# Performance work log

Hardware: AMD Instinct MI355X
Metric: run time of the kernel (lower is better)

The kernel has to match this reference:

```python
import jax, jax.numpy as jnp
import numpy as np

C = 512        # num_channels
HEADS = 8      # num_channels // num_head_channels
DH = 64        # num_head_channels
G = 32         # num_groups
EPS = 1e-5
SCALE = DH ** -0.25  # pre-multiplied into q and k (scale applied twice -> 1/sqrt(DH))


def setup_inputs() -> dict:
    key = jax.random.key(0)
    ks = jax.random.split(key, 10)
    B, H, W = 2, 64, 64
    def w(k):
        return jax.random.normal(k, (C, C), jnp.float32) * 0.02
    def b(k):
        return jax.random.normal(k, (C,), jnp.float32) * 0.02
    return {
        "x": jax.random.normal(ks[0], (B, C, H, W), jnp.float32),
        "gn_w": jnp.ones((C,), jnp.float32),
        "gn_b": jnp.zeros((C,), jnp.float32),
        "wq": w(ks[1]), "bq": b(ks[2]),
        "wk": w(ks[3]), "bk": b(ks[4]),
        "wv": w(ks[5]), "bv": b(ks[6]),
        "wp": w(ks[7]), "bp": b(ks[8]),
    }


def reference(x, gn_w, gn_b, wq, bq, wk, bk, wv, bv, wp, bp):
    B, Cc, H, W = x.shape
    # GroupNorm over (C/G, H, W) per group
    xr = x.reshape(B, G, Cc // G, H * W)
    mean = xr.mean(axis=(2, 3), keepdims=True)
    var = xr.var(axis=(2, 3), keepdims=True)
    h = ((xr - mean) * jax.lax.rsqrt(var + EPS)).reshape(B, Cc, H, W)
    h = h * gn_w[None, :, None, None] + gn_b[None, :, None, None]
    # B C H W -> B (H W) C
    t = h.reshape(B, Cc, H * W).transpose(0, 2, 1)
    # q/k pre-multiplied by SCALE (equivalent to pre_multiply_weights_by_scale)
    q = (t @ wq.T + bq) * SCALE
    k = (t @ wk.T + bk) * SCALE
    v = t @ wv.T + bv
    def split_heads(a):  # B HW (h d) -> B h HW d
        return a.reshape(B, H * W, HEADS, DH).transpose(0, 2, 1, 3)
    q, k, v = split_heads(q), split_heads(k), split_heads(v)
    # full HWxHW score matrix, softmax over keys
    attn = jax.nn.softmax(jnp.einsum('bhqd,bhkd->bhqk', q, k), axis=-1)
    o = jnp.einsum('bhqk,bhkd->bhqd', attn, v)
    o = o.transpose(0, 2, 1, 3).reshape(B, H * W, Cc)  # join heads
    o = o @ wp.T + bp
    # B (H W) C -> B C H W, residual
    return o.transpose(0, 2, 1).reshape(B, Cc, H, W) + x
```

## Files before the change

kernel.cpp:

```cpp
#include <hip/hip_runtime.h>

#define HWN 4096
#define CCH 512
#define NHEAD 8
#define DHD 64
#define NBATCH 2
#define QK_SCALE 0.35355339059327373f
#define LOG2E    1.4426950408889634f

using floatx4 = __attribute__((ext_vector_type(4))) float;
using bf16x8  = __attribute__((ext_vector_type(8))) short;
using bf16x4  = __attribute__((ext_vector_type(4))) short;

__device__ __forceinline__ unsigned short f2b(float f) {
  union { float f; unsigned u; } x; x.f = f;
  unsigned r = x.u + 0x7FFFu + ((x.u >> 16) & 1u);
  return (unsigned short)(r >> 16);
}

__device__ __forceinline__ float fast_exp2(float x) {
#if __has_builtin(__builtin_amdgcn_exp2f)
  return __builtin_amdgcn_exp2f(x);
#else
  return __expf(x * 0.69314718056f);
#endif
}

__device__ __forceinline__ unsigned pack_bf16_trunc(float lo, float hi) {
  return __builtin_amdgcn_perm(__float_as_uint(hi), __float_as_uint(lo), 0x07060302u);
}

__global__ __launch_bounds__(256) void gn_stats(const float* __restrict__ x,
                                                float* __restrict__ stat) {
  int bg = blockIdx.x;
  const float4* p = (const float4*)(x + (size_t)bg * 65536) + blockIdx.y * 2048;
  float s = 0.f, ss = 0.f;
  for (int i = threadIdx.x; i < 2048; i += 256) {
    float4 v = p[i];
    s  += v.x + v.y + v.z + v.w;
    ss += v.x*v.x + v.y*v.y + v.z*v.z + v.w*v.w;
  }
  for (int off = 32; off; off >>= 1) {
    s  += __shfl_xor(s, off);
    ss += __shfl_xor(ss, off);
  }
  __shared__ float red[8];
  int w = threadIdx.x >> 6;
  if ((threadIdx.x & 63) == 0) { red[w] = s; red[4 + w] = ss; }
  __syncthreads();
  if (threadIdx.x == 0) {
    float S  = red[0] + red[1] + red[2] + red[3];
    float SS = red[4] + red[5] + red[6] + red[7];
    atomicAdd(&stat[bg], S);
    atomicAdd(&stat[64 + bg], SS);
  }
}

__global__ __launch_bounds__(256) void prep_w(
    const float* __restrict__ wq, const float* __restrict__ wk,
    const float* __restrict__ wv, const float* __restrict__ wp,
    const float* __restrict__ bq, const float* __restrict__ bk,
    const float* __restrict__ bv,
    unsigned short* __restrict__ Wqkv, unsigned short* __restrict__ Wp,
    float* __restrict__ bqkv) {
  int i = blockIdx.x * 256 + threadIdx.x;
  if (i < 786432) {
    int row = i >> 9;
    float v;
    if (row < 512)       v = wq[i] * (QK_SCALE * LOG2E);
    else if (row < 1024) v = wk[i - 262144] * QK_SCALE;
    else                 v = wv[i - 524288];
    Wqkv[i] = f2b(v);
  } else if (i < 1048576) {
    Wp[i - 786432] = f2b(wp[i - 786432]);
  } else if (i < 1050112) {
    int j = i - 1048576;
    float v = (j < 512) ? bq[j] * (QK_SCALE * LOG2E)
            : (j < 1024) ? bk[j - 512] * QK_SCALE
            : bv[j - 1024];
    bqkv[j] = v;
  }
}

__global__ __launch_bounds__(256) void gn_apply(
    const float* __restrict__ x, const float* __restrict__ stat,
    const float* __restrict__ gnw, const float* __restrict__ gnb,
    unsigned short* __restrict__ t) {
  int pt = blockIdx.x & 63;
  int ct = (blockIdx.x >> 6) & 7;
  int b  = blockIdx.x >> 9;
  int c0 = ct * 64, p0 = pt * 64;
  __shared__ float tile[64][68];
  int tid = threadIdx.x;
  for (int pp = 0; pp < 4; ++pp) {
    int f = (pp * 256 + tid) * 4;
    int cl = f >> 6, pl = f & 63;
    int c = c0 + cl;
    float4 v = *(const float4*)(x + ((size_t)(b * 512 + c)) * 4096 + p0 + pl);
    int g = c >> 4;
    float S    = stat[b * 32 + g];
    float SS   = stat[64 + b * 32 + g];
    float mean = S * (1.f / 65536.f);
    float var  = SS * (1.f / 65536.f) - mean * mean;
    float rstd = rsqrtf(var + 1e-5f);
    float w  = gnw[c] * rstd;
    float bb = gnb[c] - mean * w;
    tile[cl][pl + 0] = v.x * w + bb;
    tile[cl][pl + 1] = v.y * w + bb;
    tile[cl][pl + 2] = v.z * w + bb;
    tile[cl][pl + 3] = v.w * w + bb;
  }
  __syncthreads();
  for (int pp = 0; pp < 2; ++pp) {
    int f = (pp * 256 + tid) * 8;
    int pl = f >> 6, cl = f & 63;
    unsigned short u[8];
#pragma unroll
    for (int j = 0; j < 8; ++j) u[j] = f2b(tile[cl + j][pl]);
    *(uint4*)(t + ((size_t)(b * 4096 + p0 + pl)) * 512 + c0 + cl) = *(uint4*)u;
  }
}

__global__ __launch_bounds__(256) void gemm_qkv(
    const unsigned short* __restrict__ t, const unsigned short* __restrict__ Wqkv,
    const float* __restrict__ bqkv,
    unsigned short* __restrict__ qo, unsigned short* __restrict__ ko,
    unsigned short* __restrict__ vo) {
  int M0 = blockIdx.x * 64;
  int N0 = blockIdx.y * 64;
  __shared__ unsigned short At[64][72];
  __shared__ unsigned short Bt[64][72];
  int tid = threadIdx.x, w = tid >> 6, l = tid & 63;
  int quad = l >> 4, m16 = l & 15;
  floatx4 acc[4] = {};
  for (int k0 = 0; k0 < 512; k0 += 64) {
    __syncthreads();
#pragma unroll
    for (int pp = 0; pp < 2; ++pp) {
      int f = (pp * 256 + tid) * 8;
      int r = f >> 6, c = f & 63;
      *(uint4*)&At[r][c] = *(const uint4*)(t    + (size_t)(M0 + r) * 512 + k0 + c);
      *(uint4*)&Bt[r][c] = *(const uint4*)(Wqkv + (size_t)(N0 + r) * 512 + k0 + c);
    }
    __syncthreads();
    bf16x8 af0 = *(const bf16x8*)&At[w * 16 + m16][quad * 8];
    bf16x8 af1 = *(const bf16x8*)&At[w * 16 + m16][32 + quad * 8];
#pragma unroll
    for (int nt = 0; nt < 4; ++nt) {
      bf16x8 b0 = *(const bf16x8*)&Bt[nt * 16 + m16][quad * 8];
      bf16x8 b1 = *(const bf16x8*)&Bt[nt * 16 + m16][32 + quad * 8];
      acc[nt] = __builtin_amdgcn_mfma_f32_16x16x32_bf16(af0, b0, acc[nt], 0, 0, 0);
      acc[nt] = __builtin_amdgcn_mfma_f32_16x16x32_bf16(af1, b1, acc[nt], 0, 0, 0);
    }
  }
  int which = N0 >> 9;
  int head  = (N0 & 511) >> 6;
  if (which == 2) {
    __syncthreads();
#pragma unroll
    for (int nt = 0; nt < 4; ++nt) {
      int d = nt * 16 + m16;
      float bias = bqkv[N0 + d];
#pragma unroll
      for (int r = 0; r < 4; ++r)
        At[d][w * 16 + quad * 4 + r] = f2b(acc[nt][r] + bias);
    }
    __syncthreads();
    int bb = M0 >> 12, p0 = M0 & 4095;
    unsigned short* dst = vo + ((size_t)(bb * 8 + head) * 64) * 4096;
#pragma unroll
    for (int pp = 0; pp < 2; ++pp) {
      int f = (pp * 256 + tid) * 8;
      int d = f >> 6, pl = f & 63;
      *(uint4*)(dst + (size_t)d * 4096 + p0 + pl) = *(uint4*)&At[d][pl];
    }
  } else {
    unsigned short* dst = (which == 0) ? qo : ko;
#pragma unroll
    for (int nt = 0; nt < 4; ++nt) {
      int n = N0 + nt * 16 + m16;
      float bias = bqkv[n];
      int d = n & 63;
#pragma unroll
      for (int r = 0; r < 4; ++r) {
        int m = M0 + w * 16 + quad * 4 + r;
        int b = m >> 12, p = m & 4095;
        dst[(((size_t)(b * 8 + head) * 4096 + p) << 6) + d] = f2b(acc[nt][r] + bias);
      }
    }
  }
}

__global__ __launch_bounds__(256, 4) void attn(
    const unsigned short* __restrict__ q, const unsigned short* __restrict__ k,
    const unsigned short* __restrict__ vt, unsigned short* __restrict__ o) {
  int qt = blockIdx.x;
  int bh = blockIdx.y;
  int b = bh >> 3, h = bh & 7;
  __shared__ unsigned short Kt[128][72];
  __shared__ unsigned short Vt[64][136];
  int tid = threadIdx.x, w = tid >> 6, l = tid & 63;
  int quad = l >> 4, m16 = l & 15;
  const size_t base = (size_t)bh * HWN * DHD;
  int krow_base = ((m16 >> 2) * 8) + (m16 & 3);

  bf16x8 qf0, qf1;
  {
    int qrow = qt * 64 + w * 16 + m16;
    const unsigned short* qp = q + base + (size_t)qrow * 64 + quad * 8;
    qf0 = *(const bf16x8*)qp;
    qf1 = *(const bf16x8*)(qp + 32);
  }
  bf16x8 ones;
#pragma unroll
  for (int z = 0; z < 8; ++z) ones[z] = (short)0x3F80;

  floatx4 accO[4] = {};
  floatx4 accL = {};
  float mrow = -1e30f;

  for (int kt = 0; kt < 32; ++kt) {
    __syncthreads();
#pragma unroll
    for (int pp = 0; pp < 4; ++pp) {
      int f = (pp * 256 + tid) * 8;
      int rk = f >> 6, ck = f & 63;
      *(uint4*)&Kt[rk][ck] = *(const uint4*)(k + base + (size_t)(kt * 128 + rk) * 64 + ck);
      int rv = f >> 7, cv = f & 127;
      *(uint4*)&Vt[rv][cv] = *(const uint4*)(vt + base + (size_t)rv * 4096 + kt * 128 + cv);
    }
    __syncthreads();
    floatx4 s[8];
#pragma unroll
    for (int nt = 0; nt < 4; ++nt)
#pragma unroll
      for (int hh = 0; hh < 2; ++hh) {
        int row = nt * 32 + hh * 4 + krow_base;
        bf16x8 kf0 = *(const bf16x8*)&Kt[row][quad * 8];
        bf16x8 kf1 = *(const bf16x8*)&Kt[row][32 + quad * 8];
        floatx4 z = {};
        z = __builtin_amdgcn_mfma_f32_16x16x32_bf16(kf0, qf0, z, 0, 0, 0);
        s[nt * 2 + hh] = __builtin_amdgcn_mfma_f32_16x16x32_bf16(kf1, qf1, z, 0, 0, 0);
      }
    float m0 = fmaxf(fmaxf(s[0][0], s[0][1]), fmaxf(s[0][2], s[0][3]));
    float m1 = fmaxf(fmaxf(s[1][0], s[1][1]), fmaxf(s[1][2], s[1][3]));
    float m2 = fmaxf(fmaxf(s[2][0], s[2][1]), fmaxf(s[2][2], s[2][3]));
    float m3 = fmaxf(fmaxf(s[3][0], s[3][1]), fmaxf(s[3][2], s[3][3]));
    float m4 = fmaxf(fmaxf(s[4][0], s[4][1]), fmaxf(s[4][2], s[4][3]));
    float m5 = fmaxf(fmaxf(s[5][0], s[5][1]), fmaxf(s[5][2], s[5][3]));
    float m6 = fmaxf(fmaxf(s[6][0], s[6][1]), fmaxf(s[6][2], s[6][3]));
    float m7 = fmaxf(fmaxf(s[7][0], s[7][1]), fmaxf(s[7][2], s[7][3]));
    float mx = fmaxf(fmaxf(fmaxf(m0, m1), fmaxf(m2, m3)),
                     fmaxf(fmaxf(m4, m5), fmaxf(m6, m7)));
    mx = fmaxf(mx, __shfl_xor(mx, 16));
    mx = fmaxf(mx, __shfl_xor(mx, 32));
    bool grew = mx > mrow;
    float mnew = fmaxf(mrow, mx);
#pragma unroll
    for (int nt = 0; nt < 8; ++nt)
#pragma unroll
      for (int i = 0; i < 4; ++i)
        s[nt][i] = fast_exp2(s[nt][i] - mnew);
    if (__ballot(grew)) {
      float alpha = fast_exp2(mrow - mnew);
      float al0 = __shfl(alpha, quad * 4 + 0);
      float al1 = __shfl(alpha, quad * 4 + 1);
      float al2 = __shfl(alpha, quad * 4 + 2);
      float al3 = __shfl(alpha, quad * 4 + 3);
#pragma unroll
      for (int dt = 0; dt < 4; ++dt) {
        accO[dt][0] *= al0; accO[dt][1] *= al1;
        accO[dt][2] *= al2; accO[dt][3] *= al3;
      }
      accL[0] *= al0; accL[1] *= al1; accL[2] *= al2; accL[3] *= al3;
    }
    mrow = mnew;
    bf16x8 pf[4];
#pragma unroll
    for (int nt = 0; nt < 4; ++nt) {
      union { unsigned u[4]; bf16x8 v; } pu;
      pu.u[0] = pack_bf16_trunc(s[nt * 2][0],     s[nt * 2][1]);
      pu.u[1] = pack_bf16_trunc(s[nt * 2][2],     s[nt * 2][3]);
      pu.u[2] = pack_bf16_trunc(s[nt * 2 + 1][0], s[nt * 2 + 1][1]);
      pu.u[3] = pack_bf16_trunc(s[nt * 2 + 1][2], s[nt * 2 + 1][3]);
      pf[nt] = pu.v;
    }
#pragma unroll
    for (int dt = 0; dt < 4; ++dt) {
#pragma unroll
      for (int nt = 0; nt < 4; ++nt) {
        bf16x8 vf = *(const bf16x8*)&Vt[dt * 16 + m16][nt * 32 + quad * 8];
        accO[dt] = __builtin_amdgcn_mfma_f32_16x16x32_bf16(pf[nt], vf, accO[dt], 0, 0, 0);
      }
    }
#pragma unroll
    for (int nt = 0; nt < 4; ++nt)
      accL = __builtin_amdgcn_mfma_f32_16x16x32_bf16(pf[nt], ones, accL, 0, 0, 0);
  }
  float li0 = 1.f / accL[0];
  float li1 = 1.f / accL[1];
  float li2 = 1.f / accL[2];
  float li3 = 1.f / accL[3];
#pragma unroll
  for (int dt = 0; dt < 4; ++dt) {
    int d = dt * 16 + m16;
    int qrow = qt * 64 + w * 16 + quad * 4;
    size_t rowb = ((size_t)(b * 4096 + qrow)) * 512 + h * 64 + d;
    o[rowb]           = f2b(accO[dt][0] * li0);
    o[rowb + 512]     = f2b(accO[dt][1] * li1);
    o[rowb + 1024]    = f2b(accO[dt][2] * li2);
    o[rowb + 1536]    = f2b(accO[dt][3] * li3);
  }
}

__global__ __launch_bounds__(256) void gemm_out(
    const unsigned short* __restrict__ o, const unsigned short* __restrict__ Wp,
    const float* __restrict__ bp, const float* __restrict__ x,
    float* __restrict__ out) {
  int C0 = blockIdx.x * 64, P0 = blockIdx.y * 64, b = blockIdx.z;
  __shared__ unsigned short At[64][72];
  __shared__ unsigned short Bt[64][72];
  int tid = threadIdx.x, w = tid >> 6, l = tid & 63;
  int quad = l >> 4, m16 = l & 15;
  floatx4 acc[4] = {};
  for (int k0 = 0; k0 < 512; k0 += 64) {
    __syncthreads();
#pragma unroll
    for (int pp = 0; pp < 2; ++pp) {
      int f = (pp * 256 + tid) * 8;
      int r = f >> 6, c = f & 63;
      *(uint4*)&At[r][c] = *(const uint4*)(Wp + (size_t)(C0 + r) * 512 + k0 + c);
      *(uint4*)&Bt[r][c] = *(const uint4*)(o + ((size_t)(b * 4096 + P0 + r)) * 512 + k0 + c);
    }
    __syncthreads();
    bf16x8 af0 = *(const bf16x8*)&At[w * 16 + m16][quad * 8];
    bf16x8 af1 = *(const bf16x8*)&At[w * 16 + m16][32 + quad * 8];
#pragma unroll
    for (int nt = 0; nt < 4; ++nt) {
      bf16x8 b0 = *(const bf16x8*)&Bt[nt * 16 + m16][quad * 8];
      bf16x8 b1 = *(const bf16x8*)&Bt[nt * 16 + m16][32 + quad * 8];
      acc[nt] = __builtin_amdgcn_mfma_f32_16x16x32_bf16(af0, b0, acc[nt], 0, 0, 0);
      acc[nt] = __builtin_amdgcn_mfma_f32_16x16x32_bf16(af1, b1, acc[nt], 0, 0, 0);
    }
  }
#pragma unroll
  for (int r = 0; r < 4; ++r) {
    int c = C0 + w * 16 + quad * 4 + r;
    float bias = bp[c];
#pragma unroll
    for (int nt = 0; nt < 4; ++nt) {
      int p = P0 + nt * 16 + m16;
      size_t idx = ((size_t)(b * 512 + c)) * 4096 + p;
      out[idx] = acc[nt][r] + bias + x[idx];
    }
  }
}

extern "C" void kernel_launch(void* const* d_in, const int* in_sizes, int n_in,
                              void* d_out, int out_size, void* d_ws, size_t ws_size,
                              hipStream_t stream) {
  const float* x   = (const float*)d_in[0];
  const float* gnw = (const float*)d_in[1];
  const float* gnb = (const float*)d_in[2];
  const float* wq  = (const float*)d_in[3];
  const float* bq  = (const float*)d_in[4];
  const float* wk  = (const float*)d_in[5];
  const float* bk  = (const float*)d_in[6];
  const float* wv  = (const float*)d_in[7];
  const float* bv  = (const float*)d_in[8];
  const float* wp  = (const float*)d_in[9];
  const float* bp  = (const float*)d_in[10];
  float* out = (float*)d_out;

  char* ws = (char*)d_ws;
  float* stat          = (float*)ws;          ws += 1024;
  float* bqkv          = (float*)ws;          ws += 8192;
  unsigned short* Wqkv = (unsigned short*)ws; ws += (size_t)1536 * 512 * 2;
  unsigned short* Wp   = (unsigned short*)ws; ws += (size_t)512 * 512 * 2;
  unsigned short* t    = (unsigned short*)ws; ws += (size_t)8192 * 512 * 2;
  unsigned short* qb   = (unsigned short*)ws; ws += (size_t)8192 * 512 * 2;
  unsigned short* kb   = (unsigned short*)ws; ws += (size_t)8192 * 512 * 2;
  unsigned short* vb   = (unsigned short*)ws; ws += (size_t)8192 * 512 * 2;
  unsigned short* ob   = (unsigned short*)ws; ws += (size_t)8192 * 512 * 2;

  hipMemsetAsync(stat, 0, 512, stream);
  dim3 g0(64, 8);
  gn_stats<<<g0, 256, 0, stream>>>(x, stat);
  prep_w<<<4103, 256, 0, stream>>>(wq, wk, wv, wp, bq, bk, bv, Wqkv, Wp, bqkv);
  gn_apply<<<1024, 256, 0, stream>>>(x, stat, gnw, gnb, t);
  dim3 g1(128, 24);
  gemm_qkv<<<g1, 256, 0, stream>>>(t, Wqkv, bqkv, qb, kb, vb);
  dim3 g2(64, 16);
  attn<<<g2, 256, 0, stream>>>(qb, kb, vb, ob);
  dim3 g3(8, 64, 2);
  gemm_out<<<g3, 256, 0, stream>>>(ob, Wp, bp, x, out);
}
```

Baseline: 274.4 us.

## Process two 16-row query tiles per wave in attention kernel

Each wave in the attention kernel now handles 32 query rows as two independent 16-row tiles, so each block covers 128 queries and the grid is halved. Every K and V tile loaded into shared memory, and every LDS fragment read, now serves twice as many queries, which cuts global and LDS traffic per query. In exchange register pressure roughly doubles, so the launch bound drops to 2 blocks per SM, and there are only 512 blocks to spread across the device, which lowers occupancy.

```diff
diff --git a/kernel.cpp b/kernel.cpp
--- a/kernel.cpp
+++ b/kernel.cpp
@@ -191,7 +191,7 @@
   }
 }
 
-__global__ __launch_bounds__(256, 4) void attn(
+__global__ __launch_bounds__(256, 2) void attn(
     const unsigned short* __restrict__ q, const unsigned short* __restrict__ k,
     const unsigned short* __restrict__ vt, unsigned short* __restrict__ o) {
   int qt = blockIdx.x;
@@ -204,20 +204,22 @@
   const size_t base = (size_t)bh * HWN * DHD;
   int krow_base = ((m16 >> 2) * 8) + (m16 & 3);
 
-  bf16x8 qf0, qf1;
+  bf16x8 qfA0, qfA1, qfB0, qfB1;
   {
-    int qrow = qt * 64 + w * 16 + m16;
+    int qrow = qt * 128 + w * 32 + m16;
     const unsigned short* qp = q + base + (size_t)qrow * 64 + quad * 8;
-    qf0 = *(const bf16x8*)qp;
-    qf1 = *(const bf16x8*)(qp + 32);
+    qfA0 = *(const bf16x8*)qp;
+    qfA1 = *(const bf16x8*)(qp + 32);
+    qfB0 = *(const bf16x8*)(qp + 16 * 64);
+    qfB1 = *(const bf16x8*)(qp + 16 * 64 + 32);
   }
   bf16x8 ones;
 #pragma unroll
   for (int z = 0; z < 8; ++z) ones[z] = (short)0x3F80;
 
-  floatx4 accO[4] = {};
-  floatx4 accL = {};
-  float mrow = -1e30f;
+  floatx4 accOA[4] = {}, accOB[4] = {};
+  floatx4 accLA = {}, accLB = {};
+  float mrowA = -1e30f, mrowB = -1e30f;
 
   for (int kt = 0; kt < 32; ++kt) {
     __syncthreads();
@@ -230,7 +232,7 @@
       *(uint4*)&Vt[rv][cv] = *(const uint4*)(vt + base + (size_t)rv * 4096 + kt * 128 + cv);
     }
     __syncthreads();
-    floatx4 s[8];
+    floatx4 sA[8], sB[8];
 #pragma unroll
     for (int nt = 0; nt < 4; ++nt)
 #pragma unroll
@@ -238,78 +240,96 @@
         int row = nt * 32 + hh * 4 + krow_base;
         bf16x8 kf0 = *(const bf16x8*)&Kt[row][quad * 8];
         bf16x8 kf1 = *(const bf16x8*)&Kt[row][32 + quad * 8];
-        floatx4 z = {};
-        z = __builtin_amdgcn_mfma_f32_16x16x32_bf16(kf0, qf0, z, 0, 0, 0);
-        s[nt * 2 + hh] = __builtin_amdgcn_mfma_f32_16x16x32_bf16(kf1, qf1, z, 0, 0, 0);
-      }
-    float m0 = fmaxf(fmaxf(s[0][0], s[0][1]), fmaxf(s[0][2], s[0][3]));
-    float m1 = fmaxf(fmaxf(s[1][0], s[1][1]), fmaxf(s[1][2], s[1][3]));
-    float m2 = fmaxf(fmaxf(s[2][0], s[2][1]), fmaxf(s[2][2], s[2][3]));
-    float m3 = fmaxf(fmaxf(s[3][0], s[3][1]), fmaxf(s[3][2], s[3][3]));
-    float m4 = fmaxf(fmaxf(s[4][0], s[4][1]), fmaxf(s[4][2], s[4][3]));
-    float m5 = fmaxf(fmaxf(s[5][0], s[5][1]), fmaxf(s[5][2], s[5][3]));
-    float m6 = fmaxf(fmaxf(s[6][0], s[6][1]), fmaxf(s[6][2], s[6][3]));
-    float m7 = fmaxf(fmaxf(s[7][0], s[7][1]), fmaxf(s[7][2], s[7][3]));
-    float mx = fmaxf(fmaxf(fmaxf(m0, m1), fmaxf(m2, m3)),
-                     fmaxf(fmaxf(m4, m5), fmaxf(m6, m7)));
-    mx = fmaxf(mx, __shfl_xor(mx, 16));
-    mx = fmaxf(mx, __shfl_xor(mx, 32));
-    bool grew = mx > mrow;
-    float mnew = fmaxf(mrow, mx);
+        floatx4 zA = {}, zB = {};
+        zA = __builtin_amdgcn_mfma_f32_16x16x32_bf16(kf0, qfA0, zA, 0, 0, 0);
+        sA[nt * 2 + hh] = __builtin_amdgcn_mfma_f32_16x16x32_bf16(kf1, qfA1, zA, 0, 0, 0);
+        zB = __builtin_amdgcn_mfma_f32_16x16x32_bf16(kf0, qfB0, zB, 0, 0, 0);
+        sB[nt * 2 + hh] = __builtin_amdgcn_mfma_f32_16x16x32_bf16(kf1, qfB1, zB, 0, 0, 0);
+      }
+    float mxA = sA[0][0], mxB = sB[0][0];
 #pragma unroll
     for (int nt = 0; nt < 8; ++nt)
 #pragma unroll
-      for (int i = 0; i < 4; ++i)
-        s[nt][i] = fast_exp2(s[nt][i] - mnew);
+      for (int i = 0; i < 4; ++i) {
+        mxA = fmaxf(mxA, sA[nt][i]);
+        mxB = fmaxf(mxB, sB[nt][i]);
+      }
+    mxA = fmaxf(mxA, __shfl_xor(mxA, 16));
+    mxA = fmaxf(mxA, __shfl_xor(mxA, 32));
+    mxB = fmaxf(mxB, __shfl_xor(mxB, 16));
+    mxB = fmaxf(mxB, __shfl_xor(mxB, 32));
+    bool grew = (mxA > mrowA) || (mxB > mrowB);
+    float mnA = fmaxf(mrowA, mxA);
+    float mnB = fmaxf(mrowB, mxB);
+#pragma unroll
+    for (int nt = 0; nt < 8; ++nt)
+#pragma unroll
+      for (int i = 0; i < 4; ++i) {
+        sA[nt][i] = fast_exp2(sA[nt][i] - mnA);
+        sB[nt][i] = fast_exp2(sB[nt][i] - mnB);
+      }
     if (__ballot(grew)) {
-      float alpha = fast_exp2(mrow - mnew);
-      float al0 = __shfl(alpha, quad * 4 + 0);
-      float al1 = __shfl(alpha, quad * 4 + 1);
-      float al2 = __shfl(alpha, quad * 4 + 2);
-      float al3 = __shfl(alpha, quad * 4 + 3);
+      float aA = fast_exp2(mrowA - mnA);
+      float aB = fast_exp2(mrowB - mnB);
+      float a0 = __shfl(aA, quad * 4 + 0), b0 = __shfl(aB, quad * 4 + 0);
+      float a1 = __shfl(aA, quad * 4 + 1), b1 = __shfl(aB, quad * 4 + 1);
+      float a2 = __shfl(aA, quad * 4 + 2), b2 = __shfl(aB, quad * 4 + 2);
+      float a3 = __shfl(aA, quad * 4 + 3), b3 = __shfl(aB, quad * 4 + 3);
 #pragma unroll
       for (int dt = 0; dt < 4; ++dt) {
-        accO[dt][0] *= al0; accO[dt][1] *= al1;
-        accO[dt][2] *= al2; accO[dt][3] *= al3;
-      }
-      accL[0] *= al0; accL[1] *= al1; accL[2] *= al2; accL[3] *= al3;
-    }
-    mrow = mnew;
-    bf16x8 pf[4];
-#pragma unroll
-    for (int nt = 0; nt < 4; ++nt) {
-      union { unsigned u[4]; bf16x8 v; } pu;
-      pu.u[0] = pack_bf16_trunc(s[nt * 2][0],     s[nt * 2][1]);
-      pu.u[1] = pack_bf16_trunc(s[nt * 2][2],     s[nt * 2][3]);
-      pu.u[2] = pack_bf16_trunc(s[nt * 2 + 1][0], s[nt * 2 + 1][1]);
-      pu.u[3] = pack_bf16_trunc(s[nt * 2 + 1][2], s[nt * 2 + 1][3]);
-      pf[nt] = pu.v;
+        accOA[dt][0] *= a0; accOA[dt][1] *= a1; accOA[dt][2] *= a2; accOA[dt][3] *= a3;
+        accOB[dt][0] *= b0; accOB[dt][1] *= b1; accOB[dt][2] *= b2; accOB[dt][3] *= b3;
+      }
+      accLA[0] *= a0; accLA[1] *= a1; accLA[2] *= a2; accLA[3] *= a3;
+      accLB[0] *= b0; accLB[1] *= b1; accLB[2] *= b2; accLB[3] *= b3;
+    }
+    mrowA = mnA; mrowB = mnB;
+    bf16x8 pfA[4], pfB[4];
+#pragma unroll
+    for (int nt = 0; nt < 4; ++nt) {
+      union { unsigned u[4]; bf16x8 v; } pa, pb;
+      pa.u[0] = pack_bf16_trunc(sA[nt * 2][0],     sA[nt * 2][1]);
+      pa.u[1] = pack_bf16_trunc(sA[nt * 2][2],     sA[nt * 2][3]);
+      pa.u[2] = pack_bf16_trunc(sA[nt * 2 + 1][0], sA[nt * 2 + 1][1]);
+      pa.u[3] = pack_bf16_trunc(sA[nt * 2 + 1][2], sA[nt * 2 + 1][3]);
+      pfA[nt] = pa.v;
+      pb.u[0] = pack_bf16_trunc(sB[nt * 2][0],     sB[nt * 2][1]);
+      pb.u[1] = pack_bf16_trunc(sB[nt * 2][2],     sB[nt * 2][3]);
+      pb.u[2] = pack_bf16_trunc(sB[nt * 2 + 1][0], sB[nt * 2 + 1][1]);
+      pb.u[3] = pack_bf16_trunc(sB[nt * 2 + 1][2], sB[nt * 2 + 1][3]);
+      pfB[nt] = pb.v;
     }
 #pragma unroll
     for (int dt = 0; dt < 4; ++dt) {
 #pragma unroll
       for (int nt = 0; nt < 4; ++nt) {
         bf16x8 vf = *(const bf16x8*)&Vt[dt * 16 + m16][nt * 32 + quad * 8];
-        accO[dt] = __builtin_amdgcn_mfma_f32_16x16x32_bf16(pf[nt], vf, accO[dt], 0, 0, 0);
-      }
-    }
-#pragma unroll
-    for (int nt = 0; nt < 4; ++nt)
-      accL = __builtin_amdgcn_mfma_f32_16x16x32_bf16(pf[nt], ones, accL, 0, 0, 0);
-  }
-  float li0 = 1.f / accL[0];
-  float li1 = 1.f / accL[1];
-  float li2 = 1.f / accL[2];
-  float li3 = 1.f / accL[3];
+        accOA[dt] = __builtin_amdgcn_mfma_f32_16x16x32_bf16(pfA[nt], vf, accOA[dt], 0, 0, 0);
+        accOB[dt] = __builtin_amdgcn_mfma_f32_16x16x32_bf16(pfB[nt], vf, accOB[dt], 0, 0, 0);
+      }
+    }
+#pragma unroll
+    for (int nt = 0; nt < 4; ++nt) {
+      accLA = __builtin_amdgcn_mfma_f32_16x16x32_bf16(pfA[nt], ones, accLA, 0, 0, 0);
+      accLB = __builtin_amdgcn_mfma_f32_16x16x32_bf16(pfB[nt], ones, accLB, 0, 0, 0);
+    }
+  }
+  float lA0 = 1.f / accLA[0], lA1 = 1.f / accLA[1], lA2 = 1.f / accLA[2], lA3 = 1.f / accLA[3];
+  float lB0 = 1.f / accLB[0], lB1 = 1.f / accLB[1], lB2 = 1.f / accLB[2], lB3 = 1.f / accLB[3];
 #pragma unroll
   for (int dt = 0; dt < 4; ++dt) {
     int d = dt * 16 + m16;
-    int qrow = qt * 64 + w * 16 + quad * 4;
-    size_t rowb = ((size_t)(b * 4096 + qrow)) * 512 + h * 64 + d;
-    o[rowb]           = f2b(accO[dt][0] * li0);
-    o[rowb + 512]     = f2b(accO[dt][1] * li1);
-    o[rowb + 1024]    = f2b(accO[dt][2] * li2);
-    o[rowb + 1536]    = f2b(accO[dt][3] * li3);
+    int qrowA = qt * 128 + w * 32 + quad * 4;
+    size_t rowb = ((size_t)(b * 4096 + qrowA)) * 512 + h * 64 + d;
+    o[rowb]           = f2b(accOA[dt][0] * lA0);
+    o[rowb + 512]     = f2b(accOA[dt][1] * lA1);
+    o[rowb + 1024]    = f2b(accOA[dt][2] * lA2);
+    o[rowb + 1536]    = f2b(accOA[dt][3] * lA3);
+    size_t rowb2 = rowb + (size_t)16 * 512;
+    o[rowb2]          = f2b(accOB[dt][0] * lB0);
+    o[rowb2 + 512]    = f2b(accOB[dt][1] * lB1);
+    o[rowb2 + 1024]   = f2b(accOB[dt][2] * lB2);
+    o[rowb2 + 1536]   = f2b(accOB[dt][3] * lB3);
   }
 }
 
@@ -390,7 +410,7 @@
   gn_apply<<<1024, 256, 0, stream>>>(x, stat, gnw, gnb, t);
   dim3 g1(128, 24);
   gemm_qkv<<<g1, 256, 0, stream>>>(t, Wqkv, bqkv, qb, kb, vb);
-  dim3 g2(64, 16);
+  dim3 g2(32, 16);
   attn<<<g2, 256, 0, stream>>>(qb, kb, vb, ob);
   dim3 g3(8, 64, 2);
   gemm_out<<<g3, 256, 0, stream>>>(ob, Wp, bp, x, out);
```

New measurement: 276.2 us. Within noise of the previous version (+0.6%).

## Split attention over two key halves and pre-swizzle K into MFMA fragment layout

Applied to the files above, without the earlier changes.

The attention kernel now splits the 4096 keys into two halves along a new grid dimension, doubling block count from 1024 to 2048. Each half writes a normalized partial output and its row max and sum, and a new merge kernel combines the halves with softmax rescaling. K is written by the QKV GEMM directly in per-lane MFMA fragment order, so attention reads K fragments from global memory instead of staging K through shared memory. The cost is an extra kernel launch, an extra round trip of partial outputs through scratch buffers (the output buffer and the t buffer are reused), and one more bf16 rounding of the partial outputs.

```diff
diff --git a/kernel.cpp b/kernel.cpp
--- a/kernel.cpp
+++ b/kernel.cpp
@@ -16,6 +16,11 @@
   union { float f; unsigned u; } x; x.f = f;
   unsigned r = x.u + 0x7FFFu + ((x.u >> 16) & 1u);
   return (unsigned short)(r >> 16);
+}
+
+__device__ __forceinline__ float b2f(unsigned short u) {
+  union { unsigned u; float f; } x; x.u = ((unsigned)u) << 16;
+  return x.f;
 }
 
 __device__ __forceinline__ float fast_exp2(float x) {
@@ -124,7 +129,7 @@
 __global__ __launch_bounds__(256) void gemm_qkv(
     const unsigned short* __restrict__ t, const unsigned short* __restrict__ Wqkv,
     const float* __restrict__ bqkv,
-    unsigned short* __restrict__ qo, unsigned short* __restrict__ ko,
+    unsigned short* __restrict__ qo, unsigned short* __restrict__ Kp,
     unsigned short* __restrict__ vo) {
   int M0 = blockIdx.x * 64;
   int N0 = blockIdx.y * 64;
@@ -174,8 +179,26 @@
       int d = f >> 6, pl = f & 63;
       *(uint4*)(dst + (size_t)d * 4096 + p0 + pl) = *(uint4*)&At[d][pl];
     }
+  } else if (which == 1) {
+    __syncthreads();
+#pragma unroll
+    for (int nt = 0; nt < 4; ++nt) {
+      float bias = bqkv[N0 + nt * 16 + m16];
+#pragma unroll
+      for (int r = 0; r < 4; ++r)
+        At[w * 16 + quad * 4 + r][nt * 16 + m16] = f2b(acc[nt][r] + bias);
+    }
+    __syncthreads();
+    int bb = M0 >> 12, p = M0 & 4095;
+    int kb = p >> 7, halfblk = (p >> 6) & 1;
+    int ig = halfblk * 4 + w;
+    int ntl = w >> 1, hh = w & 1;
+    int row = ntl * 32 + hh * 4 + ((m16 >> 2) << 3) + (m16 & 3);
+    size_t dstb = (((size_t)(bb * 8 + head) * 32 + kb) * 8 + ig) * 1024;
+#pragma unroll
+    for (int pp = 0; pp < 2; ++pp)
+      *(uint4*)(Kp + dstb + pp * 512 + l * 8) = *(uint4*)&At[row][pp * 32 + quad * 8];
   } else {
-    unsigned short* dst = (which == 0) ? qo : ko;
 #pragma unroll
     for (int nt = 0; nt < 4; ++nt) {
       int n = N0 + nt * 16 + m16;
@@ -184,30 +207,30 @@
 #pragma unroll
       for (int r = 0; r < 4; ++r) {
         int m = M0 + w * 16 + quad * 4 + r;
-        int b = m >> 12, p = m & 4095;
-        dst[(((size_t)(b * 8 + head) * 4096 + p) << 6) + d] = f2b(acc[nt][r] + bias);
+        int b = m >> 12, pp2 = m & 4095;
+        qo[(((size_t)(b * 8 + head) * 4096 + pp2) << 6) + d] = f2b(acc[nt][r] + bias);
       }
     }
   }
 }
 
 __global__ __launch_bounds__(256, 4) void attn(
-    const unsigned short* __restrict__ q, const unsigned short* __restrict__ k,
-    const unsigned short* __restrict__ vt, unsigned short* __restrict__ o) {
+    const unsigned short* __restrict__ q, const unsigned short* __restrict__ Kp,
+    const unsigned short* __restrict__ vt,
+    unsigned short* __restrict__ pO, float* __restrict__ mlbuf) {
   int qt = blockIdx.x;
   int bh = blockIdx.y;
-  int b = bh >> 3, h = bh & 7;
-  __shared__ unsigned short Kt[128][72];
+  int ks = blockIdx.z;
   __shared__ unsigned short Vt[64][136];
   int tid = threadIdx.x, w = tid >> 6, l = tid & 63;
   int quad = l >> 4, m16 = l & 15;
-  const size_t base = (size_t)bh * HWN * DHD;
-  int krow_base = ((m16 >> 2) * 8) + (m16 & 3);
+  const size_t vbase = (size_t)bh * HWN * DHD;
+  const int key0 = ks * 2048;
 
   bf16x8 qf0, qf1;
   {
     int qrow = qt * 64 + w * 16 + m16;
-    const unsigned short* qp = q + base + (size_t)qrow * 64 + quad * 8;
+    const unsigned short* qp = q + vbase + (size_t)qrow * 64 + quad * 8;
     qf0 = *(const bf16x8*)qp;
     qf1 = *(const bf16x8*)(qp + 32);
   }
@@ -219,48 +242,40 @@
   floatx4 accL = {};
   float mrow = -1e30f;
 
-  for (int kt = 0; kt < 32; ++kt) {
+  for (int kt = 0; kt < 16; ++kt) {
+    int kb = ks * 16 + kt;
     __syncthreads();
 #pragma unroll
     for (int pp = 0; pp < 4; ++pp) {
       int f = (pp * 256 + tid) * 8;
-      int rk = f >> 6, ck = f & 63;
-      *(uint4*)&Kt[rk][ck] = *(const uint4*)(k + base + (size_t)(kt * 128 + rk) * 64 + ck);
       int rv = f >> 7, cv = f & 127;
-      *(uint4*)&Vt[rv][cv] = *(const uint4*)(vt + base + (size_t)rv * 4096 + kt * 128 + cv);
-    }
-    __syncthreads();
+      *(uint4*)&Vt[rv][cv] = *(const uint4*)(vt + vbase + (size_t)rv * 4096 + key0 + kt * 128 + cv);
+    }
+    __syncthreads();
+    const unsigned short* kpb = Kp + (((size_t)bh * 32 + kb) * 8) * 1024 + l * 8;
     floatx4 s[8];
 #pragma unroll
-    for (int nt = 0; nt < 4; ++nt)
-#pragma unroll
-      for (int hh = 0; hh < 2; ++hh) {
-        int row = nt * 32 + hh * 4 + krow_base;
-        bf16x8 kf0 = *(const bf16x8*)&Kt[row][quad * 8];
-        bf16x8 kf1 = *(const bf16x8*)&Kt[row][32 + quad * 8];
-        floatx4 z = {};
-        z = __builtin_amdgcn_mfma_f32_16x16x32_bf16(kf0, qf0, z, 0, 0, 0);
-        s[nt * 2 + hh] = __builtin_amdgcn_mfma_f32_16x16x32_bf16(kf1, qf1, z, 0, 0, 0);
-      }
-    float m0 = fmaxf(fmaxf(s[0][0], s[0][1]), fmaxf(s[0][2], s[0][3]));
-    float m1 = fmaxf(fmaxf(s[1][0], s[1][1]), fmaxf(s[1][2], s[1][3]));
-    float m2 = fmaxf(fmaxf(s[2][0], s[2][1]), fmaxf(s[2][2], s[2][3]));
-    float m3 = fmaxf(fmaxf(s[3][0], s[3][1]), fmaxf(s[3][2], s[3][3]));
-    float m4 = fmaxf(fmaxf(s[4][0], s[4][1]), fmaxf(s[4][2], s[4][3]));
-    float m5 = fmaxf(fmaxf(s[5][0], s[5][1]), fmaxf(s[5][2], s[5][3]));
-    float m6 = fmaxf(fmaxf(s[6][0], s[6][1]), fmaxf(s[6][2], s[6][3]));
-    float m7 = fmaxf(fmaxf(s[7][0], s[7][1]), fmaxf(s[7][2], s[7][3]));
-    float mx = fmaxf(fmaxf(fmaxf(m0, m1), fmaxf(m2, m3)),
-                     fmaxf(fmaxf(m4, m5), fmaxf(m6, m7)));
+    for (int ig = 0; ig < 8; ++ig) {
+      bf16x8 kf0 = *(const bf16x8*)(kpb + ig * 1024);
+      bf16x8 kf1 = *(const bf16x8*)(kpb + ig * 1024 + 512);
+      floatx4 z = {};
+      z = __builtin_amdgcn_mfma_f32_16x16x32_bf16(kf0, qf0, z, 0, 0, 0);
+      s[ig] = __builtin_amdgcn_mfma_f32_16x16x32_bf16(kf1, qf1, z, 0, 0, 0);
+    }
+    float mx = s[0][0];
+#pragma unroll
+    for (int ig = 0; ig < 8; ++ig)
+#pragma unroll
+      for (int i = 0; i < 4; ++i) mx = fmaxf(mx, s[ig][i]);
     mx = fmaxf(mx, __shfl_xor(mx, 16));
     mx = fmaxf(mx, __shfl_xor(mx, 32));
     bool grew = mx > mrow;
     float mnew = fmaxf(mrow, mx);
 #pragma unroll
-    for (int nt = 0; nt < 8; ++nt)
+    for (int ig = 0; ig < 8; ++ig)
 #pragma unroll
       for (int i = 0; i < 4; ++i)
-        s[nt][i] = fast_exp2(s[nt][i] - mnew);
+        s[ig][i] = fast_exp2(s[ig][i] - mnew);
     if (__ballot(grew)) {
       float alpha = fast_exp2(mrow - mnew);
       float al0 = __shfl(alpha, quad * 4 + 0);
@@ -297,6 +312,7 @@
     for (int nt = 0; nt < 4; ++nt)
       accL = __builtin_amdgcn_mfma_f32_16x16x32_bf16(pf[nt], ones, accL, 0, 0, 0);
   }
+  const size_t prow = (size_t)(ks * 16 + bh) * 4096;
   float li0 = 1.f / accL[0];
   float li1 = 1.f / accL[1];
   float li2 = 1.f / accL[2];
@@ -305,12 +321,53 @@
   for (int dt = 0; dt < 4; ++dt) {
     int d = dt * 16 + m16;
     int qrow = qt * 64 + w * 16 + quad * 4;
-    size_t rowb = ((size_t)(b * 4096 + qrow)) * 512 + h * 64 + d;
-    o[rowb]           = f2b(accO[dt][0] * li0);
-    o[rowb + 512]     = f2b(accO[dt][1] * li1);
-    o[rowb + 1024]    = f2b(accO[dt][2] * li2);
-    o[rowb + 1536]    = f2b(accO[dt][3] * li3);
-  }
+    size_t rb = (prow + qrow) * 64 + d;
+    pO[rb]       = f2b(accO[dt][0] * li0);
+    pO[rb + 64]  = f2b(accO[dt][1] * li1);
+    pO[rb + 128] = f2b(accO[dt][2] * li2);
+    pO[rb + 192] = f2b(accO[dt][3] * li3);
+  }
+  if (m16 < 4) {
+    float mv = __shfl(mrow, quad * 4 + m16);
+    float lv = (m16 == 0) ? accL[0] : (m16 == 1) ? accL[1] : (m16 == 2) ? accL[2] : accL[3];
+    int qrow = qt * 64 + w * 16 + quad * 4 + m16;
+    float2 v; v.x = mv; v.y = lv;
+    ((float2*)mlbuf)[prow + qrow] = v;
+  }
+}
+
+__global__ __launch_bounds__(256) void attn_merge(
+    const unsigned short* __restrict__ pO, const float* __restrict__ mlbuf,
+    unsigned short* __restrict__ ob) {
+  int r = blockIdx.x * 64 + (threadIdx.x >> 2);
+  int dseg = (threadIdx.x & 3) * 16;
+  int bh = r >> 12, qq = r & 4095;
+  int b = bh >> 3, h = bh & 7;
+  const float2* mlp = (const float2*)mlbuf;
+  float2 ml0 = mlp[r];
+  float2 ml1 = mlp[65536 + r];
+  float ms = fmaxf(ml0.x, ml1.x);
+  float s0 = fast_exp2(ml0.x - ms) * ml0.y;
+  float s1 = fast_exp2(ml1.x - ms) * ml1.y;
+  float inv = 1.f / (s0 + s1);
+  float w0 = s0 * inv, w1 = s1 * inv;
+  const unsigned short* p0 = pO + ((size_t)r * 64 + dseg);
+  const unsigned short* p1 = p0 + (size_t)65536 * 64;
+  uint4 u0a = *(const uint4*)p0, u0b = *(const uint4*)(p0 + 8);
+  uint4 u1a = *(const uint4*)p1, u1b = *(const uint4*)(p1 + 8);
+  const unsigned short* a0 = (const unsigned short*)&u0a;
+  const unsigned short* a1 = (const unsigned short*)&u1a;
+  const unsigned short* b0p = (const unsigned short*)&u0b;
+  const unsigned short* b1p = (const unsigned short*)&u1b;
+  unsigned short u[16];
+#pragma unroll
+  for (int z = 0; z < 8; ++z) {
+    u[z]     = f2b(w0 * b2f(a0[z])  + w1 * b2f(a1[z]));
+    u[8 + z] = f2b(w0 * b2f(b0p[z]) + w1 * b2f(b1p[z]));
+  }
+  unsigned short* op = ob + ((size_t)(b * 4096 + qq)) * 512 + h * 64 + dseg;
+  *(uint4*)op       = *(uint4*)u;
+  *(uint4*)(op + 8) = *(uint4*)(u + 8);
 }
 
 __global__ __launch_bounds__(256) void gemm_out(
@@ -379,9 +436,12 @@
   unsigned short* Wp   = (unsigned short*)ws; ws += (size_t)512 * 512 * 2;
   unsigned short* t    = (unsigned short*)ws; ws += (size_t)8192 * 512 * 2;
   unsigned short* qb   = (unsigned short*)ws; ws += (size_t)8192 * 512 * 2;
-  unsigned short* kb   = (unsigned short*)ws; ws += (size_t)8192 * 512 * 2;
+  unsigned short* Kp   = (unsigned short*)ws; ws += (size_t)8192 * 512 * 2;
   unsigned short* vb   = (unsigned short*)ws; ws += (size_t)8192 * 512 * 2;
   unsigned short* ob   = (unsigned short*)ws; ws += (size_t)8192 * 512 * 2;
+
+  unsigned short* pO  = (unsigned short*)d_out;
+  float* mlbuf        = (float*)t;
 
   hipMemsetAsync(stat, 0, 512, stream);
   dim3 g0(64, 8);
@@ -389,9 +449,10 @@
   prep_w<<<4103, 256, 0, stream>>>(wq, wk, wv, wp, bq, bk, bv, Wqkv, Wp, bqkv);
   gn_apply<<<1024, 256, 0, stream>>>(x, stat, gnw, gnb, t);
   dim3 g1(128, 24);
-  gemm_qkv<<<g1, 256, 0, stream>>>(t, Wqkv, bqkv, qb, kb, vb);
-  dim3 g2(64, 16);
-  attn<<<g2, 256, 0, stream>>>(qb, kb, vb, ob);
+  gemm_qkv<<<g1, 256, 0, stream>>>(t, Wqkv, bqkv, qb, Kp, vb);
+  dim3 g2(64, 16, 2);
+  attn<<<g2, 256, 0, stream>>>(qb, Kp, vb, pO, mlbuf);
+  attn_merge<<<1024, 256, 0, stream>>>(pO, mlbuf, ob);
   dim3 g3(8, 64, 2);
   gemm_out<<<g3, 256, 0, stream>>>(ob, Wp, bp, x, out);
 }
```

New measurement: 255.0 us. -7.1%, faster.
